# Optimization experiments

Hardware: AMD Instinct MI355X
Metric: run time of the kernel (lower is better)

The kernel has to match this reference:

```python
import jax, jax.numpy as jnp
import numpy as np

B, T, M, P, N2 = 16, 8192, 128, 128, 128  # N2 = N//2 complex modes

def setup_inputs() -> dict:
    key = jax.random.key(0)
    k1, k2, k3, k4, k5 = jax.random.split(key, 5)
    u = jax.random.normal(k1, (B, T, M), dtype=jnp.float32)
    # log-parametrized Lambda (S5 'log' convention): Lambda = -exp(row0) + 1j*row1
    log_re = jnp.log(jax.random.uniform(k2, (N2,), minval=0.1, maxval=1.0))
    im = jnp.pi * jnp.arange(N2, dtype=jnp.float32)  # HiPPO-like imaginary spread
    Lambda_param = jnp.stack([log_re, im], axis=0).astype(jnp.float32)
    B_param = jax.random.normal(k3, (2, N2, M), dtype=jnp.float32) / np.sqrt(M)
    C_param = jax.random.normal(k4, (2, P, N2), dtype=jnp.float32) / np.sqrt(N2)
    delta = jnp.array([0.01], dtype=jnp.float32)  # default_\u0394
    return {"u": u, "Lambda_param": Lambda_param, "B_param": B_param,
            "C_param": C_param, "delta": delta}

def reference(u, Lambda_param, B_param, C_param, delta):
    # Reconstruct complex continuous-time matrices
    Lam = (-jnp.exp(Lambda_param[0]) + 1j * Lambda_param[1]).astype(jnp.complex64)   # (N2,)
    Bc = (B_param[0] + 1j * B_param[1]).astype(jnp.complex64)                        # (N2, M)
    Cc = (C_param[0] + 1j * C_param[1]).astype(jnp.complex64)                        # (P, N2)
    d = delta[0]
    # ZOH discretization: Lambda_d = exp(Lam*d), Bd = ((Lambda_d - 1)/Lam) * B
    Ld = jnp.exp(Lam * d)                                                            # (N2,)
    Bd = ((Ld - 1.0) / Lam)[:, None] * Bc                                            # (N2, M)
    # Input projection: Bu[b,t,n] = sum_m u[b,t,m] * Bd[n,m]
    Bu = jnp.einsum('btm,nm->btn', u.astype(jnp.complex64), Bd)                      # (B,T,N2)
    # Parallel scan of x_{k+1} = Ld * x_k + Bu_k, x_0 = 0 -> x holds x_1..x_T
    A = jnp.broadcast_to(Ld, Bu.shape)
    def comb(e1, e2):
        a1, b1 = e1
        a2, b2 = e2
        return (a1 * a2, a2 * b1 + b2)
    _, x = jax.lax.associative_scan(comb, (A, Bu), axis=1)                           # (B,T,N2)
    # return_next_y=True: y_k = 2*Re(C x_{k+1})
    y = 2.0 * jnp.real(jnp.einsum('btn,pn->btp', x, Cc))                             # (B,T,P)
    return y
```

## Files before the change

kernel.cpp:

```cpp
#include <hip/hip_runtime.h>
#include <hip/hip_bf16.h>

#define LCH 128
#define NCH 64
#define NCHUNKS 1024

typedef __attribute__((ext_vector_type(8))) short short8v;
typedef __attribute__((ext_vector_type(4))) short short4v;
typedef __attribute__((ext_vector_type(4))) float f32x4;

#define W2_LDINV 0
#define W2_LDP   16384
#define W2_E     32768
#define W2_CIN   163840
#define WS_WPACK_BYTE  2359296
#define WS_CCPACK_BYTE (2359296 + 65536)
#define WS_BUS_BYTE    (2359296 + 131072)
#define WS_NEED ((size_t)WS_BUS_BYTE + (size_t)NCHUNKS * 65536)

#define BUS_BYTE(s, np) ((((s) >> 3) * 4096) + ((np) * 16) + (((s) & 7) * 2))

__device__ inline unsigned short f2bf(float f) {
    union { __hip_bfloat16 h; unsigned short u; } v;
    v.h = __float2bfloat16(f);
    return v.u;
}
__device__ inline short4v pack4(float a, float b, float c, float d) {
    union { __hip_bfloat162 h2[2]; short4v s4; } pk;
    pk.h2[0] = __float22bfloat162_rn(make_float2(a, b));
    pk.h2[1] = __float22bfloat162_rn(make_float2(c, d));
    return pk.s4;
}

__global__ void k0_all(const float* __restrict__ lp, const float* __restrict__ bp,
                       const float* __restrict__ cp, const float* __restrict__ delta,
                       float2* __restrict__ ws2, unsigned short* __restrict__ wpack,
                       unsigned short* __restrict__ ccpack) {
    const int r = blockIdx.x;
    const int tid = threadIdx.x;
    if (r < 128) {
        if (tid < 256) {
            const int n = tid & 127;
            const double d = (double)delta[0];
            const double lre = -exp((double)lp[n]);
            const double lim = (double)lp[128 + n];
            const double kk = (double)(r + 1) * d;
            if (tid < 128) {
                const double mag = exp(-lre * kk);
                ws2[W2_LDINV + r * 128 + n] = make_float2((float)(mag * cos(lim * kk)),
                                                          (float)(-mag * sin(lim * kk)));
            } else {
                const double mag = exp(lre * kk);
                ws2[W2_LDP + r * 128 + n] = make_float2((float)(mag * cos(lim * kk)),
                                                        (float)(mag * sin(lim * kk)));
            }
        }
    } else if (r < 192) {
        const int gid = (r - 128) * 512 + tid;
        const int j = gid & 7;
        const int lane = (gid >> 3) & 63;
        const int ks = (gid >> 9) & 3;
        const int ntile = gid >> 11;
        const int np = ntile * 16 + (lane & 15);
        const int m = ks * 32 + ((lane >> 4) & 3) * 8 + j;
        const int n = np & 127;
        const double d = (double)delta[0];
        const double lre = -exp((double)lp[n]);
        const double lim = (double)lp[128 + n];
        const double er = exp(lre * d);
        const double ldr = er * cos(lim * d), ldi = er * sin(lim * d);
        const double nr = ldr - 1.0, ni = ldi;
        const double den = lre * lre + lim * lim;
        const double cr = (nr * lre + ni * lim) / den;
        const double ci = (ni * lre - nr * lim) / den;
        const double br = (double)bp[n * 128 + m];
        const double bi = (double)bp[16384 + n * 128 + m];
        const double v = (np < 128) ? (cr * br - ci * bi) : (cr * bi + ci * br);
        wpack[gid] = f2bf((float)v);
    } else {
        const int gid = (r - 192) * 512 + tid;
        const int j = gid & 7;
        const int lane = (gid >> 3) & 63;
        const int ks = (gid >> 9) & 7;
        const int ptile = gid >> 12;
        const int p = ptile * 16 + (lane & 15);
        const int k = ks * 32 + ((lane >> 4) & 3) * 8 + j;
        const int n = k >> 1;
        const float v = ((k & 1) == 0) ? 2.0f * cp[p * 128 + n]
                                       : -2.0f * cp[16384 + p * 128 + n];
        ccpack[gid] = f2bf(v);
    }
}

__device__ inline void stage_u(const float* __restrict__ uchunk, unsigned short* lds_u) {
    const float4* uf = (const float4*)uchunk;
    const int tid = threadIdx.x;
#pragma unroll
    for (int it = 0; it < 8; ++it) {
        const int f4 = it * 512 + tid;
        const float4 v = uf[f4];
        const int t = f4 >> 5;
        const int m = (f4 & 31) * 4;
        const int byte = (t * 256 + m * 2) ^ ((t & 7) << 4);
        *(short4v*)((char*)lds_u + byte) = pack4(v.x, v.y, v.z, v.w);
    }
}

__global__ __launch_bounds__(512, 4) void k3a_bus(const float* __restrict__ u,
                                                  float2* __restrict__ ws2,
                                                  const unsigned short* __restrict__ wpack,
                                                  char* __restrict__ busg) {
    __shared__ unsigned short lds_u[16384];
    const int tid = threadIdx.x;
    const int lane = tid & 63;
    const int w = tid >> 6;
    const int tl = lane & 15;
    const int gq = (lane >> 4) & 3;
    const int g = blockIdx.x;
    const int b = g >> 6;
    const int c = g & 63;
    const int n = w * 16 + tl;
    const short8v* wp = (const short8v*)wpack;
    char* busc = busg + (size_t)g * 65536;
    const float4* uf = (const float4*)(u + (size_t)(b * 8192 + c * 128) * 128);

    {
        float4 p0 = uf[tid], p1 = uf[512 + tid], p2 = uf[1024 + tid], p3 = uf[1536 + tid];
#pragma unroll
        for (int it = 0; it < 4; ++it) {
            const float4 v = (it == 0) ? p0 : (it == 1) ? p1 : (it == 2) ? p2 : p3;
            const int f4 = it * 512 + tid;
            const int t = f4 >> 5;
            const int m = (f4 & 31) * 4;
            const int byte = (t * 256 + m * 2) ^ ((t & 7) << 4);
            *(short4v*)((char*)lds_u + byte) = pack4(v.x, v.y, v.z, v.w);
        }
    }
    float4 q0 = uf[2048 + tid], q1 = uf[2560 + tid], q2 = uf[3072 + tid], q3 = uf[3584 + tid];
    __builtin_amdgcn_sched_barrier(0);
    __syncthreads();

    float er = 0.f, ei = 0.f;

    {
        f32x4 acc[4][2];
#pragma unroll
        for (int i = 0; i < 4; ++i) { acc[i][0] = (f32x4)0.f; acc[i][1] = (f32x4)0.f; }
        __builtin_amdgcn_s_setprio(1);
#pragma unroll
        for (int ks = 0; ks < 4; ++ks) {
            const short8v b0 = wp[(w * 4 + ks) * 64 + lane];
            const short8v b1 = wp[((8 + w) * 4 + ks) * 64 + lane];
#pragma unroll
            for (int tt2 = 0; tt2 < 4; ++tt2) {
                const int t = tt2 * 16 + tl;
                const int byte = (t * 256 + (ks * 32 + gq * 8) * 2) ^ ((t & 7) << 4);
                const short8v a = *(const short8v*)((const char*)lds_u + byte);
                acc[tt2][0] = __builtin_amdgcn_mfma_f32_16x16x32_bf16(a, b0, acc[tt2][0], 0, 0, 0);
                acc[tt2][1] = __builtin_amdgcn_mfma_f32_16x16x32_bf16(a, b1, acc[tt2][1], 0, 0, 0);
            }
        }
        __builtin_amdgcn_s_setprio(0);
#pragma unroll
        for (int tt2 = 0; tt2 < 4; ++tt2) {
            float vr[4], vi[4];
#pragma unroll
            for (int reg = 0; reg < 4; ++reg) {
                const int rr = tt2 * 16 + gq * 4 + reg;
                const float2 li = ws2[W2_LDINV + rr * 128 + n];
                const float br = acc[tt2][0][reg], bi = acc[tt2][1][reg];
                vr[reg] = li.x * br - li.y * bi;
                vi[reg] = li.x * bi + li.y * br;
                er += vr[reg];
                ei += vi[reg];
            }
            const int s0 = tt2 * 16 + gq * 4;
            const int rowr = w * 16 + tl;
            const int rowi = 128 + rowr;
            *(short4v*)(busc + BUS_BYTE(s0, rowr)) = pack4(vr[0], vr[1], vr[2], vr[3]);
            *(short4v*)(busc + BUS_BYTE(s0, rowi)) = pack4(vi[0], vi[1], vi[2], vi[3]);
        }
    }

    {
#pragma unroll
        for (int it = 0; it < 4; ++it) {
            const float4 v = (it == 0) ? q0 : (it == 1) ? q1 : (it == 2) ? q2 : q3;
            const int f4 = 2048 + it * 512 + tid;
            const int t = f4 >> 5;
            const int m = (f4 & 31) * 4;
            const int byte = (t * 256 + m * 2) ^ ((t & 7) << 4);
            *(short4v*)((char*)lds_u + byte) = pack4(v.x, v.y, v.z, v.w);
        }
    }
    __syncthreads();

    {
        f32x4 acc[4][2];
#pragma unroll
        for (int i = 0; i < 4; ++i) { acc[i][0] = (f32x4)0.f; acc[i][1] = (f32x4)0.f; }
        __builtin_amdgcn_s_setprio(1);
#pragma unroll
        for (int ks = 0; ks < 4; ++ks) {
            const short8v b0 = wp[(w * 4 + ks) * 64 + lane];
            const short8v b1 = wp[((8 + w) * 4 + ks) * 64 + lane];
#pragma unroll
            for (int tt2 = 0; tt2 < 4; ++tt2) {
                const int t = (4 + tt2) * 16 + tl;
                const int byte = (t * 256 + (ks * 32 + gq * 8) * 2) ^ ((t & 7) << 4);
                const short8v a = *(const short8v*)((const char*)lds_u + byte);
                acc[tt2][0] = __builtin_amdgcn_mfma_f32_16x16x32_bf16(a, b0, acc[tt2][0], 0, 0, 0);
                acc[tt2][1] = __builtin_amdgcn_mfma_f32_16x16x32_bf16(a, b1, acc[tt2][1], 0, 0, 0);
            }
        }
        __builtin_amdgcn_s_setprio(0);
#pragma unroll
        for (int tt2 = 0; tt2 < 4; ++tt2) {
            float vr[4], vi[4];
#pragma unroll
            for (int reg = 0; reg < 4; ++reg) {
                const int rr = (4 + tt2) * 16 + gq * 4 + reg;
                const float2 li = ws2[W2_LDINV + rr * 128 + n];
                const float br = acc[tt2][0][reg], bi = acc[tt2][1][reg];
                vr[reg] = li.x * br - li.y * bi;
                vi[reg] = li.x * bi + li.y * br;
                er += vr[reg];
                ei += vi[reg];
            }
            const int s0 = (4 + tt2) * 16 + gq * 4;
            const int rowr = w * 16 + tl;
            const int rowi = 128 + rowr;
            *(short4v*)(busc + BUS_BYTE(s0, rowr)) = pack4(vr[0], vr[1], vr[2], vr[3]);
            *(short4v*)(busc + BUS_BYTE(s0, rowi)) = pack4(vi[0], vi[1], vi[2], vi[3]);
        }
    }

    er += __shfl_xor(er, 16); ei += __shfl_xor(ei, 16);
    er += __shfl_xor(er, 32); ei += __shfl_xor(ei, 32);
    const float2 ld = ws2[W2_LDP + 127 * 128 + n];
    if (lane < 16) {
        ws2[W2_E + g * 128 + n] = make_float2(ld.x * er - ld.y * ei,
                                              ld.x * ei + ld.y * er);
    }
}

__global__ void k2_carry(float2* __restrict__ ws2) {
    const int idx = blockIdx.x * 256 + threadIdx.x;
    const int b = idx >> 7;
    const int n = idx & 127;
    const float2 l = ws2[W2_LDP + 127 * 128 + n];
    float cr = 0.f, ci = 0.f;
    for (int c = 0; c < NCH; ++c) {
        const int o = (b * NCH + c) * 128 + n;
        ws2[W2_CIN + o] = make_float2(cr, ci);
        const float2 e = ws2[W2_E + o];
        const float nr = fmaf(l.x, cr, fmaf(-l.y, ci, e.x));
        const float ni = fmaf(l.x, ci, fmaf(l.y, cr, e.y));
        cr = nr; ci = ni;
    }
}

__global__ __launch_bounds__(512, 4) void k3b_out(const float2* __restrict__ ws2,
                                                  const char* __restrict__ busg,
                                                  const unsigned short* __restrict__ ccpack,
                                                  float* __restrict__ y) {
    __shared__ unsigned short lds[32768];
    const int tid = threadIdx.x;
    const int lane = tid & 63;
    const int w = tid >> 6;
    const int tl = lane & 15;
    const int gq = (lane >> 4) & 3;
    const int g = blockIdx.x;
    const int b = g >> 6;
    const int c = g & 63;
    const int n = w * 16 + tl;
    const short8v* cc8 = (const short8v*)ccpack;
    const char* busc = busg + (size_t)g * 65536;

    short8v ONES, D0, D1;
#pragma unroll
    for (int j = 0; j < 8; ++j) {
        const int sl = gq * 8 + j;
        ONES[j] = (short)0x3F80;
        D0[j] = (sl <= tl) ? (short)0x3F80 : (short)0;
        D1[j] = (sl <= tl + 16) ? (short)0x3F80 : (short)0;
    }
    f32x4 z[8][2];
#pragma unroll
    for (int i = 0; i < 8; ++i) { z[i][0] = (f32x4)0.f; z[i][1] = (f32x4)0.f; }
    __builtin_amdgcn_s_setprio(1);
#pragma unroll
    for (int ks = 0; ks < 4; ++ks) {
        const int sb = ks * 32 + gq * 8;
        const int rowr = w * 16 + tl;
        const int rowi = 128 + rowr;
        const short8v b0 = *(const short8v*)(busc + BUS_BYTE(sb, rowr));
        const short8v b1 = *(const short8v*)(busc + BUS_BYTE(sb, rowi));
#pragma unroll
        for (int tt = 0; tt < 8; ++tt) {
            if (tt < 2 * ks) continue;
            const short8v a = (tt == 2 * ks) ? D0 : ((tt == 2 * ks + 1) ? D1 : ONES);
            z[tt][0] = __builtin_amdgcn_mfma_f32_16x16x32_bf16(a, b0, z[tt][0], 0, 0, 0);
            z[tt][1] = __builtin_amdgcn_mfma_f32_16x16x32_bf16(a, b1, z[tt][1], 0, 0, 0);
        }
    }
    __builtin_amdgcn_s_setprio(0);

    const float2 cin = ws2[W2_CIN + g * 128 + n];
#pragma unroll
    for (int tt = 0; tt < 8; ++tt) {
#pragma unroll
        for (int reg = 0; reg < 4; ++reg) {
            const int r = tt * 16 + gq * 4 + reg;
            const float2 ld = ws2[W2_LDP + r * 128 + n];
            const float zr = z[tt][0][reg] + cin.x;
            const float zi = z[tt][1][reg] + cin.y;
            const float xr = ld.x * zr - ld.y * zi;
            const float xi = ld.x * zi + ld.y * zr;
            union { __hip_bfloat162 h2; unsigned uu; } pk;
            pk.h2 = __float22bfloat162_rn(make_float2(xr, xi));
            const int byte = (r * 512 + n * 4) ^ ((r & 7) << 4);
            *(unsigned*)((char*)lds + byte) = pk.uu;
        }
    }
    __syncthreads();

    f32x4 yac[8];
#pragma unroll
    for (int i = 0; i < 8; ++i) yac[i] = (f32x4)0.f;
    __builtin_amdgcn_s_setprio(1);
#pragma unroll
    for (int ks = 0; ks < 8; ++ks) {
        const short8v bfrg = cc8[(w * 8 + ks) * 64 + lane];
#pragma unroll
        for (int tt = 0; tt < 8; ++tt) {
            const int t = tt * 16 + tl;
            const int byte = (t * 512 + (ks * 32 + gq * 8) * 2) ^ ((t & 7) << 4);
            const short8v a = *(const short8v*)((const char*)lds + byte);
            yac[tt] = __builtin_amdgcn_mfma_f32_16x16x32_bf16(a, bfrg, yac[tt], 0, 0, 0);
        }
    }
    __builtin_amdgcn_s_setprio(0);

    __syncthreads();
    const int p = w * 16 + tl;
#pragma unroll
    for (int tt = 0; tt < 8; ++tt) {
#pragma unroll
        for (int reg = 0; reg < 4; ++reg) {
            const int t = tt * 16 + gq * 4 + reg;
            const int byte = (t * 512 + p * 4) ^ ((t & 7) << 4);
            *(float*)((char*)lds + byte) = yac[tt][reg];
        }
    }
    __syncthreads();
    float4* yf = (float4*)(y + (size_t)(b * 8192 + c * 128) * 128);
#pragma unroll
    for (int it = 0; it < 8; ++it) {
        const int f4 = it * 512 + tid;
        const int row = f4 >> 5;
        const int col = (f4 & 31) * 4;
        const int byte = (row * 512 + col * 4) ^ ((row & 7) << 4);
        yf[f4] = *(float4*)((char*)lds + byte);
    }
}

__global__ __launch_bounds__(512, 4) void k1_end(const float* __restrict__ u,
                                                 float2* __restrict__ ws2,
                                                 const unsigned short* __restrict__ wpack) {
    __shared__ unsigned short lds_u[16384];
    const int tid = threadIdx.x;
    const int lane = tid & 63;
    const int w = tid >> 6;
    const int tl = lane & 15;
    const int gq = (lane >> 4) & 3;
    const int g = blockIdx.x;
    const int b = g >> 6;
    const int c = g & 63;
    const int n = w * 16 + tl;
    stage_u(u + (size_t)(b * 8192 + c * 128) * 128, lds_u);
    __syncthreads();
    const short8v* wp = (const short8v*)wpack;
    float er = 0.f, ei = 0.f;
#pragma unroll
    for (int h = 0; h < 2; ++h) {
        f32x4 acc[4][2];
#pragma unroll
        for (int i = 0; i < 4; ++i) { acc[i][0] = (f32x4)0.f; acc[i][1] = (f32x4)0.f; }
        __builtin_amdgcn_s_setprio(1);
#pragma unroll
        for (int ks = 0; ks < 4; ++ks) {
            const short8v b0 = wp[(w * 4 + ks) * 64 + lane];
            const short8v b1 = wp[((8 + w) * 4 + ks) * 64 + lane];
#pragma unroll
            for (int tt2 = 0; tt2 < 4; ++tt2) {
                const int t = (h * 4 + tt2) * 16 + tl;
                const int byte = (t * 256 + (ks * 32 + gq * 8) * 2) ^ ((t & 7) << 4);
                const short8v a = *(const short8v*)((const char*)lds_u + byte);
                acc[tt2][0] = __builtin_amdgcn_mfma_f32_16x16x32_bf16(a, b0, acc[tt2][0], 0, 0, 0);
                acc[tt2][1] = __builtin_amdgcn_mfma_f32_16x16x32_bf16(a, b1, acc[tt2][1], 0, 0, 0);
            }
        }
        __builtin_amdgcn_s_setprio(0);
        __builtin_amdgcn_sched_barrier(0);
#pragma unroll
        for (int tt2 = 0; tt2 < 4; ++tt2) {
#pragma unroll
            for (int reg = 0; reg < 4; ++reg) {
                const int r = (h * 4 + tt2) * 16 + gq * 4 + reg;
                const float2 li = ws2[W2_LDINV + r * 128 + n];
                const float br = acc[tt2][0][reg], bi = acc[tt2][1][reg];
                er += li.x * br - li.y * bi;
                ei += li.x * bi + li.y * br;
            }
        }
        __builtin_amdgcn_sched_barrier(0);
    }
    er += __shfl_xor(er, 16); ei += __shfl_xor(ei, 16);
    er += __shfl_xor(er, 32); ei += __shfl_xor(ei, 32);
    const float2 ld = ws2[W2_LDP + 127 * 128 + n];
    if (lane < 16) {
        ws2[W2_E + g * 128 + n] = make_float2(ld.x * er - ld.y * ei,
                                              ld.x * ei + ld.y * er);
    }
}

__global__ __launch_bounds__(512, 4) void k3_main(const float* __restrict__ u,
                                                  const float2* __restrict__ ws2,
                                                  const unsigned short* __restrict__ wpack,
                                                  const unsigned short* __restrict__ ccpack,
                                                  float* __restrict__ y) {
    __shared__ unsigned short lds[32768];
    const int tid = threadIdx.x;
    const int lane = tid & 63;
    const int w = tid >> 6;
    const int tl = lane & 15;
    const int gq = (lane >> 4) & 3;
    const int g = blockIdx.x;
    const int b = g >> 6;
    const int c = g & 63;
    const int n = w * 16 + tl;
    const short8v* wp = (const short8v*)wpack;
    const short8v* cc8 = (const short8v*)ccpack;

    stage_u(u + (size_t)(b * 8192 + c * 128) * 128, lds);
    __syncthreads();
#pragma unroll
    for (int hh = 0; hh < 2; ++hh) {
        const int h = 1 - hh;
        f32x4 acc[4][2];
#pragma unroll
        for (int i = 0; i < 4; ++i) { acc[i][0] = (f32x4)0.f; acc[i][1] = (f32x4)0.f; }
        __builtin_amdgcn_s_setprio(1);
#pragma unroll
        for (int ks = 0; ks < 4; ++ks) {
            const short8v b0 = wp[(w * 4 + ks) * 64 + lane];
            const short8v b1 = wp[((8 + w) * 4 + ks) * 64 + lane];
#pragma unroll
            for (int tt2 = 0; tt2 < 4; ++tt2) {
                const int t = (h * 4 + tt2) * 16 + tl;
                const int byte = (t * 256 + (ks * 32 + gq * 8) * 2) ^ ((t & 7) << 4);
                const short8v a = *(const short8v*)((const char*)lds + byte);
                acc[tt2][0] = __builtin_amdgcn_mfma_f32_16x16x32_bf16(a, b0, acc[tt2][0], 0, 0, 0);
                acc[tt2][1] = __builtin_amdgcn_mfma_f32_16x16x32_bf16(a, b1, acc[tt2][1], 0, 0, 0);
            }
        }
        __builtin_amdgcn_s_setprio(0);
        __builtin_amdgcn_sched_barrier(0);
        if (h == 0) __syncthreads();
#pragma unroll
        for (int tt2 = 0; tt2 < 4; ++tt2) {
            float vr[4], vi[4];
#pragma unroll
            for (int reg = 0; reg < 4; ++reg) {
                const int r = (h * 4 + tt2) * 16 + gq * 4 + reg;
                const float2 li = ws2[W2_LDINV + r * 128 + n];
                const float br = acc[tt2][0][reg], bi = acc[tt2][1][reg];
                vr[reg] = li.x * br - li.y * bi;
                vi[reg] = li.x * bi + li.y * br;
            }
            const int s0 = (h * 4 + tt2) * 16 + gq * 4;
            const int rowr = w * 16 + tl;
            const int rowi = 128 + rowr;
            *(short4v*)((char*)lds + BUS_BYTE(s0, rowr)) = pack4(vr[0], vr[1], vr[2], vr[3]);
            *(short4v*)((char*)lds + BUS_BYTE(s0, rowi)) = pack4(vi[0], vi[1], vi[2], vi[3]);
        }
        __builtin_amdgcn_sched_barrier(0);
    }
    short8v ONES, D0, D1;
#pragma unroll
    for (int j = 0; j < 8; ++j) {
        const int sl = gq * 8 + j;
        ONES[j] = (short)0x3F80;
        D0[j] = (sl <= tl) ? (short)0x3F80 : (short)0;
        D1[j] = (sl <= tl + 16) ? (short)0x3F80 : (short)0;
    }
    f32x4 z[8][2];
#pragma unroll
    for (int i = 0; i < 8; ++i) { z[i][0] = (f32x4)0.f; z[i][1] = (f32x4)0.f; }
#pragma unroll
    for (int ks = 0; ks < 4; ++ks) {
        const int sb = ks * 32 + gq * 8;
        const int rowr = w * 16 + tl;
        const int rowi = 128 + rowr;
        const short8v b0 = *(const short8v*)((const char*)lds + BUS_BYTE(sb, rowr));
        const short8v b1 = *(const short8v*)((const char*)lds + BUS_BYTE(sb, rowi));
#pragma unroll
        for (int tt = 0; tt < 8; ++tt) {
            if (tt < 2 * ks) continue;
            const short8v a = (tt == 2 * ks) ? D0 : ((tt == 2 * ks + 1) ? D1 : ONES);
            z[tt][0] = __builtin_amdgcn_mfma_f32_16x16x32_bf16(a, b0, z[tt][0], 0, 0, 0);
            z[tt][1] = __builtin_amdgcn_mfma_f32_16x16x32_bf16(a, b1, z[tt][1], 0, 0, 0);
        }
    }
    __syncthreads();
    const float2 cin = ws2[W2_CIN + g * 128 + n];
#pragma unroll
    for (int tt = 0; tt < 8; ++tt) {
#pragma unroll
        for (int reg = 0; reg < 4; ++reg) {
            const int r = tt * 16 + gq * 4 + reg;
            const float2 ld = ws2[W2_LDP + r * 128 + n];
            const float zr = z[tt][0][reg] + cin.x;
            const float zi = z[tt][1][reg] + cin.y;
            const float xr = ld.x * zr - ld.y * zi;
            const float xi = ld.x * zi + ld.y * zr;
            union { __hip_bfloat162 h2; unsigned uu; } pk;
            pk.h2 = __float22bfloat162_rn(make_float2(xr, xi));
            const int byte = (r * 512 + n * 4) ^ ((r & 7) << 4);
            *(unsigned*)((char*)lds + byte) = pk.uu;
        }
    }
    __syncthreads();
    f32x4 yac[8];
#pragma unroll
    for (int i = 0; i < 8; ++i) yac[i] = (f32x4)0.f;
    __builtin_amdgcn_s_setprio(1);
#pragma unroll
    for (int ks = 0; ks < 8; ++ks) {
        const short8v bfrg = cc8[(w * 8 + ks) * 64 + lane];
#pragma unroll
        for (int tt = 0; tt < 8; ++tt) {
            const int t = tt * 16 + tl;
            const int byte = (t * 512 + (ks * 32 + gq * 8) * 2) ^ ((t & 7) << 4);
            const short8v a = *(const short8v*)((const char*)lds + byte);
            yac[tt] = __builtin_amdgcn_mfma_f32_16x16x32_bf16(a, bfrg, yac[tt], 0, 0, 0);
        }
    }
    __builtin_amdgcn_s_setprio(0);
    const int p = w * 16 + tl;
    float* yrow = y + (size_t)(b * 8192 + c * 128) * 128;
#pragma unroll
    for (int tt = 0; tt < 8; ++tt) {
#pragma unroll
        for (int reg = 0; reg < 4; ++reg) {
            const int t = tt * 16 + gq * 4 + reg;
            yrow[t * 128 + p] = yac[tt][reg];
        }
    }
}

extern "C" void kernel_launch(void* const* d_in, const int* in_sizes, int n_in,
                              void* d_out, int out_size, void* d_ws, size_t ws_size,
                              hipStream_t stream) {
    const float* u     = (const float*)d_in[0];
    const float* lp    = (const float*)d_in[1];
    const float* bp    = (const float*)d_in[2];
    const float* cp    = (const float*)d_in[3];
    const float* delta = (const float*)d_in[4];
    float* y  = (float*)d_out;
    float2* ws2 = (float2*)d_ws;
    unsigned short* wpack  = (unsigned short*)((char*)d_ws + WS_WPACK_BYTE);
    unsigned short* ccpack = (unsigned short*)((char*)d_ws + WS_CCPACK_BYTE);
    char* busg = (char*)d_ws + WS_BUS_BYTE;

    k0_all<<<256, 512, 0, stream>>>(lp, bp, cp, delta, ws2, wpack, ccpack);

    if (ws_size >= WS_NEED) {
        k3a_bus <<<NCHUNKS, 512, 0, stream>>>(u, ws2, wpack, busg);
        k2_carry<<<8, 256, 0, stream>>>(ws2);
        k3b_out <<<NCHUNKS, 512, 0, stream>>>(ws2, busg, ccpack, y);
    } else {
        k1_end  <<<NCHUNKS, 512, 0, stream>>>(u, ws2, wpack);
        k2_carry<<<8, 256, 0, stream>>>(ws2);
        k3_main <<<NCHUNKS, 512, 0, stream>>>(u, ws2, wpack, ccpack, y);
    }
}
```

Baseline: 84.49 us.

## Split k3b intra-chunk scan into halves, raise occupancy, store outputs directly

The intra-chunk prefix-sum MFMA stage in k3b_out is split into two halves of four row tiles each, so only half the accumulators are live at once. Launch bounds go from 4 to 6 waves per EU to allow more resident blocks. The final output write no longer stages through LDS with two barriers; each thread writes its accumulator values straight to global memory. In exchange, the second half redoes the bus fragment loads for ks 0 and 1, and the direct stores are narrower scalar stores that are less coalesced than the previous float4 writes.

```diff
diff --git a/kernel.cpp b/kernel.cpp
--- a/kernel.cpp
+++ b/kernel.cpp
@@ -260,7 +260,7 @@
     }
 }
 
-__global__ __launch_bounds__(512, 4) void k3b_out(const float2* __restrict__ ws2,
+__global__ __launch_bounds__(512, 6) void k3b_out(const float2* __restrict__ ws2,
                                                   const char* __restrict__ busg,
                                                   const unsigned short* __restrict__ ccpack,
                                                   float* __restrict__ y) {
@@ -285,42 +285,82 @@
         D0[j] = (sl <= tl) ? (short)0x3F80 : (short)0;
         D1[j] = (sl <= tl + 16) ? (short)0x3F80 : (short)0;
     }
-    f32x4 z[8][2];
-#pragma unroll
-    for (int i = 0; i < 8; ++i) { z[i][0] = (f32x4)0.f; z[i][1] = (f32x4)0.f; }
-    __builtin_amdgcn_s_setprio(1);
-#pragma unroll
-    for (int ks = 0; ks < 4; ++ks) {
-        const int sb = ks * 32 + gq * 8;
-        const int rowr = w * 16 + tl;
-        const int rowi = 128 + rowr;
-        const short8v b0 = *(const short8v*)(busc + BUS_BYTE(sb, rowr));
-        const short8v b1 = *(const short8v*)(busc + BUS_BYTE(sb, rowi));
-#pragma unroll
-        for (int tt = 0; tt < 8; ++tt) {
-            if (tt < 2 * ks) continue;
-            const short8v a = (tt == 2 * ks) ? D0 : ((tt == 2 * ks + 1) ? D1 : ONES);
-            z[tt][0] = __builtin_amdgcn_mfma_f32_16x16x32_bf16(a, b0, z[tt][0], 0, 0, 0);
-            z[tt][1] = __builtin_amdgcn_mfma_f32_16x16x32_bf16(a, b1, z[tt][1], 0, 0, 0);
-        }
-    }
-    __builtin_amdgcn_s_setprio(0);
-
     const float2 cin = ws2[W2_CIN + g * 128 + n];
-#pragma unroll
-    for (int tt = 0; tt < 8; ++tt) {
-#pragma unroll
-        for (int reg = 0; reg < 4; ++reg) {
-            const int r = tt * 16 + gq * 4 + reg;
-            const float2 ld = ws2[W2_LDP + r * 128 + n];
-            const float zr = z[tt][0][reg] + cin.x;
-            const float zi = z[tt][1][reg] + cin.y;
-            const float xr = ld.x * zr - ld.y * zi;
-            const float xi = ld.x * zi + ld.y * zr;
-            union { __hip_bfloat162 h2; unsigned uu; } pk;
-            pk.h2 = __float22bfloat162_rn(make_float2(xr, xi));
-            const int byte = (r * 512 + n * 4) ^ ((r & 7) << 4);
-            *(unsigned*)((char*)lds + byte) = pk.uu;
+    const int rowr = w * 16 + tl;
+    const int rowi = 128 + rowr;
+
+    {
+        f32x4 z[4][2];
+#pragma unroll
+        for (int i = 0; i < 4; ++i) { z[i][0] = (f32x4)0.f; z[i][1] = (f32x4)0.f; }
+        __builtin_amdgcn_s_setprio(1);
+#pragma unroll
+        for (int ks = 0; ks < 2; ++ks) {
+            const int sb = ks * 32 + gq * 8;
+            const short8v b0 = *(const short8v*)(busc + BUS_BYTE(sb, rowr));
+            const short8v b1 = *(const short8v*)(busc + BUS_BYTE(sb, rowi));
+#pragma unroll
+            for (int tt = 0; tt < 4; ++tt) {
+                if (tt < 2 * ks) continue;
+                const short8v a = (tt == 2 * ks) ? D0 : ((tt == 2 * ks + 1) ? D1 : ONES);
+                z[tt][0] = __builtin_amdgcn_mfma_f32_16x16x32_bf16(a, b0, z[tt][0], 0, 0, 0);
+                z[tt][1] = __builtin_amdgcn_mfma_f32_16x16x32_bf16(a, b1, z[tt][1], 0, 0, 0);
+            }
+        }
+        __builtin_amdgcn_s_setprio(0);
+#pragma unroll
+        for (int tt = 0; tt < 4; ++tt) {
+#pragma unroll
+            for (int reg = 0; reg < 4; ++reg) {
+                const int r = tt * 16 + gq * 4 + reg;
+                const float2 ld = ws2[W2_LDP + r * 128 + n];
+                const float zr = z[tt][0][reg] + cin.x;
+                const float zi = z[tt][1][reg] + cin.y;
+                const float xr = ld.x * zr - ld.y * zi;
+                const float xi = ld.x * zi + ld.y * zr;
+                union { __hip_bfloat162 h2; unsigned uu; } pk;
+                pk.h2 = __float22bfloat162_rn(make_float2(xr, xi));
+                const int byte = (r * 512 + n * 4) ^ ((r & 7) << 4);
+                *(unsigned*)((char*)lds + byte) = pk.uu;
+            }
+        }
+    }
+
+    {
+        f32x4 z[4][2];
+#pragma unroll
+        for (int i = 0; i < 4; ++i) { z[i][0] = (f32x4)0.f; z[i][1] = (f32x4)0.f; }
+        __builtin_amdgcn_s_setprio(1);
+#pragma unroll
+        for (int ks = 0; ks < 4; ++ks) {
+            const int sb = ks * 32 + gq * 8;
+            const short8v b0 = *(const short8v*)(busc + BUS_BYTE(sb, rowr));
+            const short8v b1 = *(const short8v*)(busc + BUS_BYTE(sb, rowi));
+#pragma unroll
+            for (int tt2 = 0; tt2 < 4; ++tt2) {
+                const int tt = 4 + tt2;
+                if (tt < 2 * ks) continue;
+                const short8v a = (tt == 2 * ks) ? D0 : ((tt == 2 * ks + 1) ? D1 : ONES);
+                z[tt2][0] = __builtin_amdgcn_mfma_f32_16x16x32_bf16(a, b0, z[tt2][0], 0, 0, 0);
+                z[tt2][1] = __builtin_amdgcn_mfma_f32_16x16x32_bf16(a, b1, z[tt2][1], 0, 0, 0);
+            }
+        }
+        __builtin_amdgcn_s_setprio(0);
+#pragma unroll
+        for (int tt2 = 0; tt2 < 4; ++tt2) {
+#pragma unroll
+            for (int reg = 0; reg < 4; ++reg) {
+                const int r = (4 + tt2) * 16 + gq * 4 + reg;
+                const float2 ld = ws2[W2_LDP + r * 128 + n];
+                const float zr = z[tt2][0][reg] + cin.x;
+                const float zi = z[tt2][1][reg] + cin.y;
+                const float xr = ld.x * zr - ld.y * zi;
+                const float xi = ld.x * zi + ld.y * zr;
+                union { __hip_bfloat162 h2; unsigned uu; } pk;
+                pk.h2 = __float22bfloat162_rn(make_float2(xr, xi));
+                const int byte = (r * 512 + n * 4) ^ ((r & 7) << 4);
+                *(unsigned*)((char*)lds + byte) = pk.uu;
+            }
         }
     }
     __syncthreads();
@@ -341,27 +381,15 @@
         }
     }
     __builtin_amdgcn_s_setprio(0);
-
-    __syncthreads();
     const int p = w * 16 + tl;
+    float* yrow = y + (size_t)(b * 8192 + c * 128) * 128;
 #pragma unroll
     for (int tt = 0; tt < 8; ++tt) {
 #pragma unroll
         for (int reg = 0; reg < 4; ++reg) {
             const int t = tt * 16 + gq * 4 + reg;
-            const int byte = (t * 512 + p * 4) ^ ((t & 7) << 4);
-            *(float*)((char*)lds + byte) = yac[tt][reg];
-        }
-    }
-    __syncthreads();
-    float4* yf = (float4*)(y + (size_t)(b * 8192 + c * 128) * 128);
-#pragma unroll
-    for (int it = 0; it < 8; ++it) {
-        const int f4 = it * 512 + tid;
-        const int row = f4 >> 5;
-        const int col = (f4 & 31) * 4;
-        const int byte = (row * 512 + col * 4) ^ ((row & 7) << 4);
-        yf[f4] = *(float4*)((char*)lds + byte);
+            yrow[t * 128 + p] = yac[tt][reg];
+        }
     }
 }
 
```

New measurement: 81.73 us (median of 2 runs). 1.03x faster.
